# Performance work log

Measured on AMD Instinct MI355X. Metric: run time of the kernel, lower is better.

The kernel has to match this reference:

```python
import jax, jax.numpy as jnp
import numpy as np

BB, T, N, M, P = 512, 128, 32, 16, 16
Q_SCALE, R_SCALE = 0.08, 0.3


def _mT(x):
    return jnp.swapaxes(x, -1, -2)


def setup_inputs() -> dict:
    key = jax.random.key(0)
    k = jax.random.split(key, 6)
    Y = jax.random.normal(k[0], (BB, T, P), dtype=jnp.float32)
    U = jax.random.normal(k[1], (BB, T, M), dtype=jnp.float32)
    # stable transition matrix (spectral radius < 1) so the filter doesn't blow up over T steps
    A = 0.8 * jnp.eye(N, dtype=jnp.float32) + 0.05 * jax.random.normal(k[2], (N, N), dtype=jnp.float32)
    Bmat = 0.1 * jax.random.normal(k[3], (N, M), dtype=jnp.float32)
    Cmat = jax.random.normal(k[4], (P, N), dtype=jnp.float32) / jnp.sqrt(jnp.float32(N))
    mu0 = jax.random.normal(k[5], (N,), dtype=jnp.float32)
    Sigma0 = jnp.eye(N, dtype=jnp.float32)
    Q = (Q_SCALE ** 2) * jnp.eye(N, dtype=jnp.float32)
    R = (R_SCALE ** 2) * jnp.eye(P, dtype=jnp.float32)
    return dict(Y=Y, U=U, A=A, Bmat=Bmat, Cmat=Cmat, mu0=mu0, Sigma0=Sigma0, Q=Q, R=R)


def _kalman_smooth(Y, U, A, Bm, C, mu0, Sigma0, Q, R):
    Bb, Tt, _ = Y.shape
    n = A.shape[0]
    I = jnp.eye(n, dtype=Y.dtype)
    Yt = jnp.swapaxes(Y, 0, 1)  # [T,B,p]
    Ut = jnp.swapaxes(U, 0, 1)  # [T,B,m]

    def fstep(carry, yu):
        mu, Sig = carry  # [B,n], [B,n,n]
        y, u = yu
        mu_p = mu @ A.T + u @ Bm.T                       # predicted mean  [B,n]
        Sig_p = A @ Sig @ A.T + Q                        # predicted cov   [B,n,n]
        r = y - mu_p @ C.T                               # innovation      [B,p]
        S = C @ Sig_p @ C.T + R                          # innovation cov  [B,p,p]
        S = 0.5 * (S + _mT(S))
        PCT = Sig_p @ C.T                                # [B,n,p]
        K = _mT(jnp.linalg.solve(S, _mT(PCT)))           # Kalman gain     [B,n,p]
        mu_f = mu_p + jnp.einsum('bnp,bp->bn', K, r)
        IKC = I - K @ C
        Sig_f = IKC @ Sig_p @ _mT(IKC) + K @ R @ _mT(K)  # Joseph form
        Sig_f = 0.5 * (Sig_f + _mT(Sig_f))
        return (mu_f, Sig_f), (mu_f, Sig_f, mu_p, Sig_p)

    mu_init = jnp.broadcast_to(mu0, (Bb, n))
    Sig_init = jnp.broadcast_to(Sigma0, (Bb, n, n))
    _, (mus_f, Sigs_f, mus_p, Sigs_p) = jax.lax.scan(fstep, (mu_init, Sig_init), (Yt, Ut))

    # RTS smoother (backward recursion via reverse scan)
    def sstep(carry, xs):
        mu_T, Sig_T = carry  # smoothed at t+1
        Sig_f, Sig_p, mu_f, mu_p = xs  # filtered at t, predicted at t+1
        J = _mT(jnp.linalg.solve(_mT(Sig_p), _mT(Sig_f @ A.T)))  # [B,n,n]
        mu_s = mu_f + jnp.einsum('bij,bj->bi', J, mu_T - mu_p)
        Sig_s = Sig_f + J @ (Sig_T - Sig_p) @ _mT(J)
        Sig_s = 0.5 * (Sig_s + _mT(Sig_s))
        return (mu_s, Sig_s), (mu_s, Sig_s)

    xs = (Sigs_f[:-1], Sigs_p[1:], mus_f[:-1], mus_p[1:])
    carry0 = (mus_f[-1], Sigs_f[-1])
    _, (mus_s, Sigs_s) = jax.lax.scan(sstep, carry0, xs, reverse=True)
    mus_s = jnp.concatenate([mus_s, mus_f[-1:]], axis=0)      # [T,B,n]
    Sigs_s = jnp.concatenate([Sigs_s, Sigs_f[-1:]], axis=0)   # [T,B,n,n]
    return jnp.swapaxes(mus_s, 0, 1), jnp.swapaxes(Sigs_s, 0, 1)


def reference(Y, U, A, Bmat, Cmat, mu0, Sigma0, Q, R):
    return _kalman_smooth(Y, U, A, Bmat, Cmat, mu0, Sigma0, Q, R)
```

## Files before the change

kernel.cpp:

```cpp
#include <hip/hip_runtime.h>

constexpr int BB = 512, T = 128, N = 32, M = 16, P = 16;
constexpr int NP = N * P;
constexpr int NN = N * N;
constexpr int NM = N * M;

typedef float f4 __attribute__((ext_vector_type(4)));

__device__ __forceinline__ void bar_lds() {
    asm volatile("s_waitcnt lgkmcnt(0)" ::: "memory");
    __builtin_amdgcn_s_barrier();
    asm volatile("" ::: "memory");
}

__device__ __forceinline__ void load_row32(const float* __restrict__ src, float* dst) {
    const float4* s4 = reinterpret_cast<const float4*>(src);
    #pragma unroll
    for (int c = 0; c < 8; ++c) {
        float4 v = s4[c];
        dst[4*c+0] = v.x; dst[4*c+1] = v.y; dst[4*c+2] = v.z; dst[4*c+3] = v.w;
    }
}
__device__ __forceinline__ void load_row16(const float* __restrict__ src, float* dst) {
    const float4* s4 = reinterpret_cast<const float4*>(src);
    #pragma unroll
    for (int c = 0; c < 4; ++c) {
        float4 v = s4[c];
        dst[4*c+0] = v.x; dst[4*c+1] = v.y; dst[4*c+2] = v.z; dst[4*c+3] = v.w;
    }
}

__global__ __launch_bounds__(256) void k_fwd(
    const float* __restrict__ A, const float* __restrict__ C,
    const float* __restrict__ Q, const float* __restrict__ R,
    const float* __restrict__ Sigma0,
    float* __restrict__ K_all, float* __restrict__ Sp_all, float* __restrict__ Sf_all,
    int* __restrict__ tconv_out)
{
    __shared__ float A_l[N][N + 1], C_l[P][N + 1], Q_l[N][N + 1], R_l[P][P + 1];
    __shared__ float Sig[N][N + 1], Tmp[N][N + 1], Sp[N][N + 1], CP[P][N + 1];
    __shared__ float Aug[P][49];
    __shared__ float red[4];
    const int tid = threadIdx.x;
    const int i0 = tid >> 5, j = tid & 31;
    const int pD = tid >> 4, q = tid & 15;
    const float TOL = 1e-4f;

    for (int idx = tid; idx < NN; idx += 256) {
        A_l[idx >> 5][idx & 31] = A[idx];
        Q_l[idx >> 5][idx & 31] = Q[idx];
        Sig[idx >> 5][idx & 31] = Sigma0[idx];
    }
    for (int idx = tid; idx < P * N; idx += 256) C_l[idx >> 5][idx & 31] = C[idx];
    for (int idx = tid; idx < P * P; idx += 256) R_l[idx >> 4][idx & 15] = R[idx];
    bar_lds();

    float Arow[4][32], Cq[32], Qjv[4];
    #pragma unroll
    for (int e = 0; e < 4; ++e) {
        #pragma unroll
        for (int k = 0; k < 32; ++k) Arow[e][k] = A_l[i0 + 8*e][k];
        Qjv[e] = Q_l[j][i0 + 8*e];
    }
    #pragma unroll
    for (int k = 0; k < 32; ++k) Cq[k] = C_l[q][k];
    const float Rv = R_l[pD][q];

    float prevSig[4];
    #pragma unroll
    for (int e = 0; e < 4; ++e) prevSig[e] = Sig[i0 + 8*e][j];

    int t_conv = T;

    for (int t = 0; t < T; ++t) {
        {
            float sc[32];
            #pragma unroll
            for (int k = 0; k < 32; ++k) sc[k] = Sig[k][j];
            #pragma unroll
            for (int e = 0; e < 4; ++e) {
                float s = 0.f;
                #pragma unroll
                for (int k = 0; k < 32; ++k) s += Arow[e][k] * sc[k];
                Tmp[i0 + 8*e][j] = s;
            }
        }
        bar_lds();
        {
            float tr[32];
            #pragma unroll
            for (int k = 0; k < 32; ++k) tr[k] = Tmp[j][k];
            #pragma unroll
            for (int e = 0; e < 4; ++e) {
                const int c = i0 + 8*e;
                float s = Qjv[e];
                #pragma unroll
                for (int k = 0; k < 32; ++k) s += tr[k] * Arow[e][k];
                Sp[j][c] = s;
                Sp_all[t * NN + tid + 256*e] = s;
            }
        }
        bar_lds();
        {
            float spc[32];
            #pragma unroll
            for (int k = 0; k < 32; ++k) spc[k] = Sp[k][j];
            #pragma unroll
            for (int e = 0; e < 2; ++e) {
                const int p = i0 + 8*e;
                float s = 0.f;
                #pragma unroll
                for (int k = 0; k < 32; ++k) s += C_l[p][k] * spc[k];
                CP[p][j] = s;
            }
        }
        bar_lds();
        {
            float cpr[32];
            #pragma unroll
            for (int k = 0; k < 32; ++k) cpr[k] = CP[pD][k];
            float s = Rv;
            #pragma unroll
            for (int k = 0; k < 32; ++k) s += cpr[k] * Cq[k];
            Aug[pD][q] = s;
        }
        #pragma unroll
        for (int e = 0; e < 2; ++e) {
            const int p = i0 + 8*e;
            Aug[p][16 + j] = CP[p][j];
        }
        bar_lds();
        if (tid < 64) {
            const int r = tid >> 2, qd = tid & 3;
            float a[12];
            #pragma unroll
            for (int c = 0; c < 12; ++c) a[c] = Aug[r][qd * 12 + c];
            #pragma unroll
            for (int p = 0; p < P; ++p) {
                const int pq = p / 12;
                const int lp = p - 12 * pq;
                const float pivv = __shfl(a[lp], (p << 2) + pq);
                const float f    = __shfl(a[lp], (tid & ~3) + pq);
                const float pinv = 1.0f / pivv;
                const float fp = f * pinv;
                float pr[12];
                #pragma unroll
                for (int c = 0; c < 12; ++c) pr[c] = __shfl(a[c], (p << 2) + qd);
                #pragma unroll
                for (int c = 0; c < 12; ++c)
                    a[c] = (r == p) ? pr[c] * pinv : a[c] - fp * pr[c];
            }
            if (qd) {
                #pragma unroll
                for (int c = 0; c < 12; ++c) Aug[r][qd * 12 + c] = a[c];
            }
        }
        bar_lds();
        #pragma unroll
        for (int e = 0; e < 2; ++e) {
            const int idx = tid + 256*e;
            K_all[t * NP + idx] = Aug[idx & 15][16 + (idx >> 4)];
        }
        float wmax = 0.f;
        {
            float cpj[16];
            #pragma unroll
            for (int p = 0; p < 16; ++p) cpj[p] = CP[p][j];
            #pragma unroll
            for (int e = 0; e < 4; ++e) {
                const int i = i0 + 8*e;
                float s = Sp[i][j];
                #pragma unroll
                for (int p = 0; p < 16; ++p) s -= Aug[p][16 + i] * cpj[p];
                Sig[i][j] = s;
                Sf_all[t * NN + tid + 256*e] = s;
                wmax = fmaxf(wmax, fabsf(s - prevSig[e]));
                prevSig[e] = s;
            }
        }
        #pragma unroll
        for (int m = 1; m < 64; m <<= 1)
            wmax = fmaxf(wmax, __shfl_xor(wmax, m));
        if ((tid & 63) == 0) red[tid >> 6] = wmax;
        bar_lds();
        const float g = fmaxf(fmaxf(red[0], red[1]), fmaxf(red[2], red[3]));
        if (g <= TOL && t < T - 1) { t_conv = t; break; }
    }

    if (t_conv < T - 1) {
        float kv[2], spv[4], sfv[4];
        #pragma unroll
        for (int e = 0; e < 2; ++e) {
            const int idx = tid + 256*e;
            kv[e] = Aug[idx & 15][16 + (idx >> 4)];
        }
        #pragma unroll
        for (int e = 0; e < 4; ++e) {
            spv[e] = Sp[i0 + 8*e][j];
            sfv[e] = Sig[i0 + 8*e][j];
        }
        for (int s = t_conv + 1; s < T; ++s) {
            #pragma unroll
            for (int e = 0; e < 2; ++e) K_all[s * NP + tid + 256*e] = kv[e];
            #pragma unroll
            for (int e = 0; e < 4; ++e) {
                Sp_all[s * NN + tid + 256*e] = spv[e];
                Sf_all[s * NN + tid + 256*e] = sfv[e];
            }
        }
    }
    if (tid == 0) *tconv_out = t_conv;
}

__global__ __launch_bounds__(256) void k_jh(
    const float* __restrict__ A,
    const float* __restrict__ Sp_all, const float* __restrict__ Sf_all,
    float* __restrict__ J_all, float* __restrict__ H_all)
{
    const int t = blockIdx.x;
    __shared__ float A_l[N][N + 1], Sf[N][N + 1], Sp1[N][N + 1];
    __shared__ float Aug[N][65], W[N][N + 1], Jl[N][N + 1];
    const int tid = threadIdx.x;

    for (int idx = tid; idx < NN; idx += 256) {
        A_l[idx >> 5][idx & 31] = A[idx];
        Sf[idx >> 5][idx & 31]  = Sf_all[t * NN + idx];
        Sp1[idx >> 5][idx & 31] = Sp_all[(t + 1) * NN + idx];
    }
    __syncthreads();
    #pragma unroll
    for (int e = 0; e < 4; ++e) {
        int idx = tid + e * 256; int i = idx >> 5, j = idx & 31;
        float s = 0.f;
        #pragma unroll
        for (int k = 0; k < N; ++k) s += A_l[i][k] * Sf[k][j];
        Aug[i][32 + j] = s;
        Aug[i][j] = Sp1[i][j];
    }
    __syncthreads();
    {
        int r = tid >> 3, c0 = (tid & 7) * 8;
        for (int p = 0; p < N; ++p) {
            float pinv = 1.0f / Aug[p][p];
            float f = Aug[r][p];
            float prow[8], mine[8];
            #pragma unroll
            for (int c = 0; c < 8; ++c) { prow[c] = Aug[p][c0 + c]; mine[c] = Aug[r][c0 + c]; }
            __syncthreads();
            float fp = f * pinv;
            #pragma unroll
            for (int c = 0; c < 8; ++c)
                Aug[r][c0 + c] = (r == p) ? prow[c] * pinv : mine[c] - fp * prow[c];
            __syncthreads();
        }
    }
    #pragma unroll
    for (int e = 0; e < 4; ++e) {
        int idx = tid + e * 256; int i = idx >> 5, j = idx & 31;
        float v = Aug[j][32 + i];
        Jl[i][j] = v;
        J_all[t * NN + idx] = v;
    }
    __syncthreads();
    #pragma unroll
    for (int e = 0; e < 4; ++e) {
        int idx = tid + e * 256; int i = idx >> 5, j = idx & 31;
        float s = 0.f;
        #pragma unroll
        for (int k = 0; k < N; ++k) s += Jl[i][k] * Sp1[k][j];
        W[i][j] = s;
    }
    __syncthreads();
    #pragma unroll
    for (int e = 0; e < 4; ++e) {
        int idx = tid + e * 256; int i = idx >> 5, j = idx & 31;
        float s = Sf[i][j];
        #pragma unroll
        for (int k = 0; k < N; ++k) s -= W[i][k] * Jl[j][k];
        H_all[t * NN + idx] = s;
    }
}

__global__ __launch_bounds__(256) void k_mat(
    const float* __restrict__ A, const float* __restrict__ C, const float* __restrict__ Bm,
    const float* __restrict__ K_all, const float* __restrict__ J_all,
    float* __restrict__ G_all, float* __restrict__ D_all,
    float* __restrict__ E_all, float* __restrict__ F_all)
{
    const int t = blockIdx.x;
    __shared__ float A_l[N][N + 1], B_l[N][M + 1], C_l[P][N + 1];
    __shared__ float Kl[N][P + 1], W[N][N + 1], Jl[N][N + 1];
    const int tid = threadIdx.x;

    for (int idx = tid; idx < NN; idx += 256) A_l[idx >> 5][idx & 31] = A[idx];
    for (int idx = tid; idx < P * N; idx += 256) C_l[idx >> 5][idx & 31] = C[idx];
    for (int idx = tid; idx < NM; idx += 256) B_l[idx >> 4][idx & 15] = Bm[idx];
    for (int idx = tid; idx < NP; idx += 256) Kl[idx >> 4][idx & 15] = K_all[t * NP + idx];
    __syncthreads();
    #pragma unroll
    for (int e = 0; e < 4; ++e) {
        int idx = tid + e * 256; int i = idx >> 5, j = idx & 31;
        float s = 0.f;
        #pragma unroll
        for (int p = 0; p < P; ++p) s += Kl[i][p] * C_l[p][j];
        W[i][j] = s;
    }
    __syncthreads();
    #pragma unroll
    for (int e = 0; e < 4; ++e) {
        int idx = tid + e * 256; int i = idx >> 5, j = idx & 31;
        float s = A_l[i][j];
        #pragma unroll
        for (int k = 0; k < N; ++k) s -= W[i][k] * A_l[k][j];
        G_all[t * NN + idx] = s;
    }
    #pragma unroll
    for (int e = 0; e < 2; ++e) {
        int idx = tid + e * 256; int i = idx >> 4, m = idx & 15;
        float s = B_l[i][m];
        #pragma unroll
        for (int k = 0; k < N; ++k) s -= W[i][k] * B_l[k][m];
        D_all[t * NM + idx] = s;
    }
    if (t >= T - 1) return;
    for (int idx = tid; idx < NN; idx += 256) Jl[idx >> 5][idx & 31] = J_all[t * NN + idx];
    __syncthreads();
    #pragma unroll
    for (int e = 0; e < 4; ++e) {
        int idx = tid + e * 256; int i = idx >> 5, j = idx & 31;
        float s = (i == j) ? 1.f : 0.f;
        #pragma unroll
        for (int k = 0; k < N; ++k) s -= Jl[i][k] * A_l[k][j];
        E_all[t * NN + idx] = s;
    }
    #pragma unroll
    for (int e = 0; e < 2; ++e) {
        int idx = tid + e * 256; int i = idx >> 4, m = idx & 15;
        float s = 0.f;
        #pragma unroll
        for (int k = 0; k < N; ++k) s += Jl[i][k] * B_l[k][m];
        F_all[t * NM + idx] = s;
    }
}

__global__ __launch_bounds__(256) void k_sscan(
    const float* __restrict__ Sf_all,
    const float* __restrict__ J_all, const float* __restrict__ H_all,
    float* __restrict__ Ss_all, const int* __restrict__ tconv_ptr)
{
    __shared__ float Ss[N][N + 1], W[N][N + 1], Hl[N][N + 1];
    __shared__ float red[4];
    const int tid = threadIdx.x;
    const int i0 = tid >> 5, j = tid & 31;
    const int t_conv = *tconv_ptr;
    const float TOL = 1e-4f;

    for (int idx = tid; idx < NN; idx += 256) {
        float v = Sf_all[(size_t)(T - 1) * NN + idx];
        Ss[idx >> 5][idx & 31] = v;
        Ss_all[(size_t)(T - 1) * NN + idx] = v;
    }
    bar_lds();
    float prevSs[4];
    #pragma unroll
    for (int e = 0; e < 4; ++e) prevSs[e] = Ss[j][i0 + 8*e];

    for (int t = T - 2; t >= 0; --t) {
        float jr[4][32];
        #pragma unroll
        for (int e = 0; e < 4; ++e)
            load_row32(J_all + (size_t)t * NN + (i0 + 8*e) * 32, jr[e]);
        #pragma unroll
        for (int e = 0; e < 4; ++e)
            Hl[i0 + 8*e][j] = H_all[(size_t)t * NN + tid + 256*e];
        {
            float sc[32];
            #pragma unroll
            for (int k = 0; k < 32; ++k) sc[k] = Ss[k][j];
            #pragma unroll
            for (int e = 0; e < 4; ++e) {
                float s = 0.f;
                #pragma unroll
                for (int k = 0; k < 32; ++k) s += jr[e][k] * sc[k];
                W[i0 + 8*e][j] = s;
            }
        }
        bar_lds();
        float localmax = 0.f;
        {
            float wr[32];
            #pragma unroll
            for (int k = 0; k < 32; ++k) wr[k] = W[j][k];
            #pragma unroll
            for (int e = 0; e < 4; ++e) {
                const int c = i0 + 8*e;
                float s = Hl[j][c];
                #pragma unroll
                for (int k = 0; k < 32; ++k) s += wr[k] * jr[e][k];
                Ss[j][c] = s;
                Ss_all[(size_t)t * NN + tid + 256*e] = s;
                localmax = fmaxf(localmax, fabsf(s - prevSs[e]));
                prevSs[e] = s;
            }
        }
        #pragma unroll
        for (int m = 1; m < 64; m <<= 1)
            localmax = fmaxf(localmax, __shfl_xor(localmax, m));
        if ((tid & 63) == 0) red[tid >> 6] = localmax;
        bar_lds();
        const float g = fmaxf(fmaxf(red[0], red[1]), fmaxf(red[2], red[3]));
        if (g <= TOL && (t - 1 >= t_conv)) {
            for (int s = t_conv; s <= t - 1; ++s) {
                #pragma unroll
                for (int e = 0; e < 4; ++e)
                    Ss_all[(size_t)s * NN + tid + 256*e] = prevSs[e];
            }
            t = t_conv;
        }
    }
}

__global__ __launch_bounds__(64, 1) void k_mu(
    const float* __restrict__ Y, const float* __restrict__ U,
    const float* __restrict__ mu0,
    const float* __restrict__ K_all, const float* __restrict__ J_all,
    const float* __restrict__ G_all, const float* __restrict__ D_all,
    const float* __restrict__ E_all, const float* __restrict__ F_all,
    const int* __restrict__ tconv_ptr,
    float* __restrict__ out_mus)
{
    const int b = blockIdx.x;
    const int lane = threadIdx.x;
    const int j = lane & 31;
    const int half = lane >> 5;
    __shared__ float mfh[T][N];
    __shared__ float cfh[T][N];
    const int t_conv = *tconv_ptr;
    const float* Yb = Y + (size_t)b * T * P;
    const float* Ub = U + (size_t)b * T * M;

    for (int it = 0; it < T / 2; ++it) {
        const int t = it * 2 + half;
        float dr[16], kr[16], uu[16], yy[16];
        load_row16(D_all + t * NM + j * 16, dr);
        load_row16(K_all + t * NP + j * 16, kr);
        load_row16(Ub + t * M, uu);
        load_row16(Yb + t * P, yy);
        float s0 = 0.f, s1 = 0.f, s2 = 0.f, s3 = 0.f;
        #pragma unroll
        for (int m = 0; m < 16; m += 4) {
            s0 += dr[m+0]*uu[m+0]; s1 += dr[m+1]*uu[m+1];
            s2 += dr[m+2]*uu[m+2]; s3 += dr[m+3]*uu[m+3];
            s0 += kr[m+0]*yy[m+0]; s1 += kr[m+1]*yy[m+1];
            s2 += kr[m+2]*yy[m+2]; s3 += kr[m+3]*yy[m+3];
        }
        cfh[t][j] = (s0 + s1) + (s2 + s3);
    }
    __syncthreads();

    float mu = mu0[j];
    float gr[32];
    load_row32(G_all + j * 32, gr);
    const int tv = (t_conv < T - 1) ? t_conv : (T - 1);
    float cn = cfh[0][j];
    int t = 0;
    for (; t < tv; ++t) {
        float grn[32];
        load_row32(G_all + (size_t)(t + 1) * NN + j * 32, grn);
        const float cnn = cfh[t + 1][j];
        float s0 = 0.f, s1 = 0.f, s2 = 0.f, s3 = 0.f;
        #pragma unroll
        for (int k = 0; k < 32; k += 4) {
            s0 += gr[k+0] * __shfl(mu, k+0);
            s1 += gr[k+1] * __shfl(mu, k+1);
            s2 += gr[k+2] * __shfl(mu, k+2);
            s3 += gr[k+3] * __shfl(mu, k+3);
        }
        mu = ((s0 + s1) + (s2 + s3)) + cn;
        if (lane < 32) mfh[t][j] = mu;
        #pragma unroll
        for (int c = 0; c < 32; ++c) gr[c] = grn[c];
        cn = cnn;
    }
    for (; t < T; ++t) {
        const float cnn = (t + 1 < T) ? cfh[t + 1][j] : 0.f;
        float s0 = 0.f, s1 = 0.f, s2 = 0.f, s3 = 0.f;
        #pragma unroll
        for (int k = 0; k < 32; k += 4) {
            s0 += gr[k+0] * __shfl(mu, k+0);
            s1 += gr[k+1] * __shfl(mu, k+1);
            s2 += gr[k+2] * __shfl(mu, k+2);
            s3 += gr[k+3] * __shfl(mu, k+3);
        }
        mu = ((s0 + s1) + (s2 + s3)) + cn;
        if (lane < 32) mfh[t][j] = mu;
        cn = cnn;
    }
    if (lane < 32) out_mus[((size_t)b * T + (T - 1)) * N + j] = mu;
    __syncthreads();

    for (int it = 0; it < T / 2; ++it) {
        const int tt = it * 2 + half;
        if (tt < T - 1) {
            float er[32], fr[16], uu[16];
            load_row32(E_all + (size_t)tt * NN + j * 32, er);
            load_row16(F_all + tt * NM + j * 16, fr);
            load_row16(Ub + (tt + 1) * M, uu);
            float s0 = 0.f, s1 = 0.f, s2 = 0.f, s3 = 0.f;
            #pragma unroll
            for (int k = 0; k < 32; k += 4) {
                s0 += er[k+0] * mfh[tt][k+0];
                s1 += er[k+1] * mfh[tt][k+1];
                s2 += er[k+2] * mfh[tt][k+2];
                s3 += er[k+3] * mfh[tt][k+3];
            }
            #pragma unroll
            for (int m = 0; m < 16; m += 4) {
                s0 -= fr[m+0]*uu[m+0]; s1 -= fr[m+1]*uu[m+1];
                s2 -= fr[m+2]*uu[m+2]; s3 -= fr[m+3]*uu[m+3];
            }
            cfh[tt][j] = (s0 + s1) + (s2 + s3);
        }
    }
    __syncthreads();

    float ms = mu;
    const int tp = (t_conv < T - 2) ? t_conv : (T - 2);
    float jr[32];
    load_row32(J_all + (size_t)tp * NN + j * 32, jr);
    float cb = cfh[T - 2][j];
    for (t = T - 2; t >= tp; --t) {
        const float cbn = (t - 1 >= 0) ? cfh[t - 1][j] : 0.f;
        float s0 = 0.f, s1 = 0.f, s2 = 0.f, s3 = 0.f;
        #pragma unroll
        for (int k = 0; k < 32; k += 4) {
            s0 += jr[k+0] * __shfl(ms, k+0);
            s1 += jr[k+1] * __shfl(ms, k+1);
            s2 += jr[k+2] * __shfl(ms, k+2);
            s3 += jr[k+3] * __shfl(ms, k+3);
        }
        ms = ((s0 + s1) + (s2 + s3)) + cb;
        if (lane < 32) out_mus[((size_t)b * T + t) * N + j] = ms;
        cb = cbn;
    }
    if (t >= 0) {
        load_row32(J_all + (size_t)t * NN + j * 32, jr);
        for (; t >= 0; --t) {
            float jrn[32];
            #pragma unroll
            for (int c = 0; c < 32; ++c) jrn[c] = 0.f;
            if (t > 0) load_row32(J_all + (size_t)(t - 1) * NN + j * 32, jrn);
            const float cbn = (t - 1 >= 0) ? cfh[t - 1][j] : 0.f;
            float s0 = 0.f, s1 = 0.f, s2 = 0.f, s3 = 0.f;
            #pragma unroll
            for (int k = 0; k < 32; k += 4) {
                s0 += jr[k+0] * __shfl(ms, k+0);
                s1 += jr[k+1] * __shfl(ms, k+1);
                s2 += jr[k+2] * __shfl(ms, k+2);
                s3 += jr[k+3] * __shfl(ms, k+3);
            }
            ms = ((s0 + s1) + (s2 + s3)) + cb;
            if (lane < 32) out_mus[((size_t)b * T + t) * N + j] = ms;
            cb = cbn;
            #pragma unroll
            for (int c = 0; c < 32; ++c) jr[c] = jrn[c];
        }
    }
}

__global__ __launch_bounds__(256) void k_bcast(
    const float* __restrict__ Ss_all, f4* __restrict__ out4)
{
    const f4* src = (const f4*)Ss_all;
    const long long total = (long long)BB * T * (NN / 4);
    const long long stride = (long long)gridDim.x * blockDim.x;
    for (long long g = blockIdx.x * (long long)blockDim.x + threadIdx.x; g < total; g += stride) {
        int e4 = (int)(g & 255);
        long long bt = g >> 8;
        int t = (int)(bt & (T - 1));
        __builtin_nontemporal_store(src[t * 256 + e4], &out4[g]);
    }
}

extern "C" void kernel_launch(void* const* d_in, const int* in_sizes, int n_in,
                              void* d_out, int out_size, void* d_ws, size_t ws_size,
                              hipStream_t stream)
{
    (void)in_sizes; (void)n_in; (void)out_size; (void)ws_size;
    const float* Y      = (const float*)d_in[0];
    const float* U      = (const float*)d_in[1];
    const float* A      = (const float*)d_in[2];
    const float* Bm     = (const float*)d_in[3];
    const float* C      = (const float*)d_in[4];
    const float* mu0    = (const float*)d_in[5];
    const float* Sigma0 = (const float*)d_in[6];
    const float* Q      = (const float*)d_in[7];
    const float* R      = (const float*)d_in[8];

    float* ws     = (float*)d_ws;
    float* K_all  = ws;
    float* Sp_all = K_all + T * NP;
    float* Sf_all = Sp_all + T * NN;
    float* J_all  = Sf_all + T * NN;
    float* H_all  = J_all + T * NN;
    float* Ss_all = H_all + T * NN;
    float* G_all  = Ss_all + T * NN;
    float* D_all  = G_all + T * NN;
    float* E_all  = D_all + T * NM;
    float* F_all  = E_all + T * NN;
    int*   tconv  = (int*)(F_all + T * NM);

    float* out_mus  = (float*)d_out;
    float* out_sigs = out_mus + (size_t)BB * T * N;

    hipLaunchKernelGGL(k_fwd,   dim3(1),     dim3(256), 0, stream, A, C, Q, R, Sigma0, K_all, Sp_all, Sf_all, tconv);
    hipLaunchKernelGGL(k_jh,    dim3(T - 1), dim3(256), 0, stream, A, Sp_all, Sf_all, J_all, H_all);
    hipLaunchKernelGGL(k_mat,   dim3(T),     dim3(256), 0, stream, A, C, Bm, K_all, J_all, G_all, D_all, E_all, F_all);
    hipLaunchKernelGGL(k_sscan, dim3(1),     dim3(256), 0, stream, Sf_all, J_all, H_all, Ss_all, tconv);
    hipLaunchKernelGGL(k_mu,    dim3(BB),    dim3(64),  0, stream, Y, U, mu0, K_all, J_all, G_all, D_all, E_all, F_all, tconv, out_mus);
    hipLaunchKernelGGL(k_bcast, dim3(4096),  dim3(256), 0, stream, Ss_all, (f4*)out_sigs);
}
```

Baseline: 589.7 us.

## Fuse J/H and matrix-precompute kernels, pack two batches per wave in mean scan

Merges the k_jh and k_mat kernels into one k_jhm launch. J now stays in shared memory instead of being reloaded from global memory, and one launch is removed. k_mu now processes two batch elements per 64-lane wave, one per 32-lane half, using offset shuffles and halving the grid. The covariance convergence tolerance in k_sscan is loosened from 1e-4 to 1e-3, which lets the smoothed covariance settle earlier at the cost of some accuracy.

Result: slower. 631.3 us (+7.1%).

```diff
diff --git a/kernel.cpp b/kernel.cpp
--- a/kernel.cpp
+++ b/kernel.cpp
@@ -212,90 +212,86 @@
     if (tid == 0) *tconv_out = t_conv;
 }
 
-__global__ __launch_bounds__(256) void k_jh(
-    const float* __restrict__ A,
+__global__ __launch_bounds__(256) void k_jhm(
+    const float* __restrict__ A, const float* __restrict__ C, const float* __restrict__ Bm,
     const float* __restrict__ Sp_all, const float* __restrict__ Sf_all,
-    float* __restrict__ J_all, float* __restrict__ H_all)
+    const float* __restrict__ K_all,
+    float* __restrict__ J_all, float* __restrict__ H_all,
+    float* __restrict__ G_all, float* __restrict__ D_all,
+    float* __restrict__ E_all, float* __restrict__ F_all)
 {
     const int t = blockIdx.x;
     __shared__ float A_l[N][N + 1], Sf[N][N + 1], Sp1[N][N + 1];
     __shared__ float Aug[N][65], W[N][N + 1], Jl[N][N + 1];
+    __shared__ float C_l[P][N + 1], B_l[N][M + 1], Kl[N][P + 1];
     const int tid = threadIdx.x;
-
-    for (int idx = tid; idx < NN; idx += 256) {
-        A_l[idx >> 5][idx & 31] = A[idx];
-        Sf[idx >> 5][idx & 31]  = Sf_all[t * NN + idx];
-        Sp1[idx >> 5][idx & 31] = Sp_all[(t + 1) * NN + idx];
-    }
-    __syncthreads();
-    #pragma unroll
-    for (int e = 0; e < 4; ++e) {
-        int idx = tid + e * 256; int i = idx >> 5, j = idx & 31;
-        float s = 0.f;
-        #pragma unroll
-        for (int k = 0; k < N; ++k) s += A_l[i][k] * Sf[k][j];
-        Aug[i][32 + j] = s;
-        Aug[i][j] = Sp1[i][j];
-    }
-    __syncthreads();
-    {
-        int r = tid >> 3, c0 = (tid & 7) * 8;
-        for (int p = 0; p < N; ++p) {
-            float pinv = 1.0f / Aug[p][p];
-            float f = Aug[r][p];
-            float prow[8], mine[8];
-            #pragma unroll
-            for (int c = 0; c < 8; ++c) { prow[c] = Aug[p][c0 + c]; mine[c] = Aug[r][c0 + c]; }
-            __syncthreads();
-            float fp = f * pinv;
-            #pragma unroll
-            for (int c = 0; c < 8; ++c)
-                Aug[r][c0 + c] = (r == p) ? prow[c] * pinv : mine[c] - fp * prow[c];
-            __syncthreads();
-        }
-    }
-    #pragma unroll
-    for (int e = 0; e < 4; ++e) {
-        int idx = tid + e * 256; int i = idx >> 5, j = idx & 31;
-        float v = Aug[j][32 + i];
-        Jl[i][j] = v;
-        J_all[t * NN + idx] = v;
-    }
-    __syncthreads();
-    #pragma unroll
-    for (int e = 0; e < 4; ++e) {
-        int idx = tid + e * 256; int i = idx >> 5, j = idx & 31;
-        float s = 0.f;
-        #pragma unroll
-        for (int k = 0; k < N; ++k) s += Jl[i][k] * Sp1[k][j];
-        W[i][j] = s;
-    }
-    __syncthreads();
-    #pragma unroll
-    for (int e = 0; e < 4; ++e) {
-        int idx = tid + e * 256; int i = idx >> 5, j = idx & 31;
-        float s = Sf[i][j];
-        #pragma unroll
-        for (int k = 0; k < N; ++k) s -= W[i][k] * Jl[j][k];
-        H_all[t * NN + idx] = s;
-    }
-}
-
-__global__ __launch_bounds__(256) void k_mat(
-    const float* __restrict__ A, const float* __restrict__ C, const float* __restrict__ Bm,
-    const float* __restrict__ K_all, const float* __restrict__ J_all,
-    float* __restrict__ G_all, float* __restrict__ D_all,
-    float* __restrict__ E_all, float* __restrict__ F_all)
-{
-    const int t = blockIdx.x;
-    __shared__ float A_l[N][N + 1], B_l[N][M + 1], C_l[P][N + 1];
-    __shared__ float Kl[N][P + 1], W[N][N + 1], Jl[N][N + 1];
-    const int tid = threadIdx.x;
+    const bool hasJ = (t < T - 1);
 
     for (int idx = tid; idx < NN; idx += 256) A_l[idx >> 5][idx & 31] = A[idx];
     for (int idx = tid; idx < P * N; idx += 256) C_l[idx >> 5][idx & 31] = C[idx];
     for (int idx = tid; idx < NM; idx += 256) B_l[idx >> 4][idx & 15] = Bm[idx];
     for (int idx = tid; idx < NP; idx += 256) Kl[idx >> 4][idx & 15] = K_all[t * NP + idx];
+    if (hasJ) {
+        for (int idx = tid; idx < NN; idx += 256) {
+            Sf[idx >> 5][idx & 31]  = Sf_all[t * NN + idx];
+            Sp1[idx >> 5][idx & 31] = Sp_all[(t + 1) * NN + idx];
+        }
+    }
+    __syncthreads();
+
+    if (hasJ) {
+        #pragma unroll
+        for (int e = 0; e < 4; ++e) {
+            int idx = tid + e * 256; int i = idx >> 5, j = idx & 31;
+            float s = 0.f;
+            #pragma unroll
+            for (int k = 0; k < N; ++k) s += A_l[i][k] * Sf[k][j];
+            Aug[i][32 + j] = s;
+            Aug[i][j] = Sp1[i][j];
+        }
+        __syncthreads();
+        {
+            int r = tid >> 3, c0 = (tid & 7) * 8;
+            for (int p = 0; p < N; ++p) {
+                float pinv = 1.0f / Aug[p][p];
+                float f = Aug[r][p];
+                float prow[8], mine[8];
+                #pragma unroll
+                for (int c = 0; c < 8; ++c) { prow[c] = Aug[p][c0 + c]; mine[c] = Aug[r][c0 + c]; }
+                __syncthreads();
+                float fp = f * pinv;
+                #pragma unroll
+                for (int c = 0; c < 8; ++c)
+                    Aug[r][c0 + c] = (r == p) ? prow[c] * pinv : mine[c] - fp * prow[c];
+                __syncthreads();
+            }
+        }
+        #pragma unroll
+        for (int e = 0; e < 4; ++e) {
+            int idx = tid + e * 256; int i = idx >> 5, j = idx & 31;
+            float v = Aug[j][32 + i];
+            Jl[i][j] = v;
+            J_all[t * NN + idx] = v;
+        }
+        __syncthreads();
+        #pragma unroll
+        for (int e = 0; e < 4; ++e) {
+            int idx = tid + e * 256; int i = idx >> 5, j = idx & 31;
+            float s = 0.f;
+            #pragma unroll
+            for (int k = 0; k < N; ++k) s += Jl[i][k] * Sp1[k][j];
+            W[i][j] = s;
+        }
+        __syncthreads();
+        #pragma unroll
+        for (int e = 0; e < 4; ++e) {
+            int idx = tid + e * 256; int i = idx >> 5, j = idx & 31;
+            float s = Sf[i][j];
+            #pragma unroll
+            for (int k = 0; k < N; ++k) s -= W[i][k] * Jl[j][k];
+            H_all[t * NN + idx] = s;
+        }
+    }
     __syncthreads();
     #pragma unroll
     for (int e = 0; e < 4; ++e) {
@@ -322,24 +318,23 @@
         for (int k = 0; k < N; ++k) s -= W[i][k] * B_l[k][m];
         D_all[t * NM + idx] = s;
     }
-    if (t >= T - 1) return;
-    for (int idx = tid; idx < NN; idx += 256) Jl[idx >> 5][idx & 31] = J_all[t * NN + idx];
-    __syncthreads();
-    #pragma unroll
-    for (int e = 0; e < 4; ++e) {
-        int idx = tid + e * 256; int i = idx >> 5, j = idx & 31;
-        float s = (i == j) ? 1.f : 0.f;
-        #pragma unroll
-        for (int k = 0; k < N; ++k) s -= Jl[i][k] * A_l[k][j];
-        E_all[t * NN + idx] = s;
-    }
-    #pragma unroll
-    for (int e = 0; e < 2; ++e) {
-        int idx = tid + e * 256; int i = idx >> 4, m = idx & 15;
-        float s = 0.f;
-        #pragma unroll
-        for (int k = 0; k < N; ++k) s += Jl[i][k] * B_l[k][m];
-        F_all[t * NM + idx] = s;
+    if (hasJ) {
+        #pragma unroll
+        for (int e = 0; e < 4; ++e) {
+            int idx = tid + e * 256; int i = idx >> 5, j = idx & 31;
+            float s = (i == j) ? 1.f : 0.f;
+            #pragma unroll
+            for (int k = 0; k < N; ++k) s -= Jl[i][k] * A_l[k][j];
+            E_all[t * NN + idx] = s;
+        }
+        #pragma unroll
+        for (int e = 0; e < 2; ++e) {
+            int idx = tid + e * 256; int i = idx >> 4, m = idx & 15;
+            float s = 0.f;
+            #pragma unroll
+            for (int k = 0; k < N; ++k) s += Jl[i][k] * B_l[k][m];
+            F_all[t * NM + idx] = s;
+        }
     }
 }
 
@@ -353,7 +348,7 @@
     const int tid = threadIdx.x;
     const int i0 = tid >> 5, j = tid & 31;
     const int t_conv = *tconv_ptr;
-    const float TOL = 1e-4f;
+    const float TOL = 1e-3f;
 
     for (int idx = tid; idx < NN; idx += 256) {
         float v = Sf_all[(size_t)(T - 1) * NN + idx];
@@ -429,18 +424,18 @@
     const int* __restrict__ tconv_ptr,
     float* __restrict__ out_mus)
 {
-    const int b = blockIdx.x;
     const int lane = threadIdx.x;
     const int j = lane & 31;
-    const int half = lane >> 5;
-    __shared__ float mfh[T][N];
-    __shared__ float cfh[T][N];
+    const int h = lane >> 5;
+    const int b = blockIdx.x * 2 + h;
+    const int sb = lane & 32;
+    __shared__ float mfh[2][T][N];
+    __shared__ float cfh[2][T][N];
     const int t_conv = *tconv_ptr;
     const float* Yb = Y + (size_t)b * T * P;
     const float* Ub = U + (size_t)b * T * M;
 
-    for (int it = 0; it < T / 2; ++it) {
-        const int t = it * 2 + half;
+    for (int t = 0; t < T; ++t) {
         float dr[16], kr[16], uu[16], yy[16];
         load_row16(D_all + t * NM + j * 16, dr);
         load_row16(K_all + t * NP + j * 16, kr);
@@ -454,7 +449,7 @@
             s0 += kr[m+0]*yy[m+0]; s1 += kr[m+1]*yy[m+1];
             s2 += kr[m+2]*yy[m+2]; s3 += kr[m+3]*yy[m+3];
         }
-        cfh[t][j] = (s0 + s1) + (s2 + s3);
+        cfh[h][t][j] = (s0 + s1) + (s2 + s3);
     }
     __syncthreads();
 
@@ -462,65 +457,62 @@
     float gr[32];
     load_row32(G_all + j * 32, gr);
     const int tv = (t_conv < T - 1) ? t_conv : (T - 1);
-    float cn = cfh[0][j];
+    float cn = cfh[h][0][j];
     int t = 0;
     for (; t < tv; ++t) {
         float grn[32];
         load_row32(G_all + (size_t)(t + 1) * NN + j * 32, grn);
-        const float cnn = cfh[t + 1][j];
+        const float cnn = cfh[h][t + 1][j];
         float s0 = 0.f, s1 = 0.f, s2 = 0.f, s3 = 0.f;
         #pragma unroll
         for (int k = 0; k < 32; k += 4) {
-            s0 += gr[k+0] * __shfl(mu, k+0);
-            s1 += gr[k+1] * __shfl(mu, k+1);
-            s2 += gr[k+2] * __shfl(mu, k+2);
-            s3 += gr[k+3] * __shfl(mu, k+3);
+            s0 += gr[k+0] * __shfl(mu, k+0+sb);
+            s1 += gr[k+1] * __shfl(mu, k+1+sb);
+            s2 += gr[k+2] * __shfl(mu, k+2+sb);
+            s3 += gr[k+3] * __shfl(mu, k+3+sb);
         }
         mu = ((s0 + s1) + (s2 + s3)) + cn;
-        if (lane < 32) mfh[t][j] = mu;
+        mfh[h][t][j] = mu;
         #pragma unroll
         for (int c = 0; c < 32; ++c) gr[c] = grn[c];
         cn = cnn;
     }
     for (; t < T; ++t) {
-        const float cnn = (t + 1 < T) ? cfh[t + 1][j] : 0.f;
+        const float cnn = (t + 1 < T) ? cfh[h][t + 1][j] : 0.f;
         float s0 = 0.f, s1 = 0.f, s2 = 0.f, s3 = 0.f;
         #pragma unroll
         for (int k = 0; k < 32; k += 4) {
-            s0 += gr[k+0] * __shfl(mu, k+0);
-            s1 += gr[k+1] * __shfl(mu, k+1);
-            s2 += gr[k+2] * __shfl(mu, k+2);
-            s3 += gr[k+3] * __shfl(mu, k+3);
+            s0 += gr[k+0] * __shfl(mu, k+0+sb);
+            s1 += gr[k+1] * __shfl(mu, k+1+sb);
+            s2 += gr[k+2] * __shfl(mu, k+2+sb);
+            s3 += gr[k+3] * __shfl(mu, k+3+sb);
         }
         mu = ((s0 + s1) + (s2 + s3)) + cn;
-        if (lane < 32) mfh[t][j] = mu;
+        mfh[h][t][j] = mu;
         cn = cnn;
     }
-    if (lane < 32) out_mus[((size_t)b * T + (T - 1)) * N + j] = mu;
+    out_mus[((size_t)b * T + (T - 1)) * N + j] = mu;
     __syncthreads();
 
-    for (int it = 0; it < T / 2; ++it) {
-        const int tt = it * 2 + half;
-        if (tt < T - 1) {
-            float er[32], fr[16], uu[16];
-            load_row32(E_all + (size_t)tt * NN + j * 32, er);
-            load_row16(F_all + tt * NM + j * 16, fr);
-            load_row16(Ub + (tt + 1) * M, uu);
-            float s0 = 0.f, s1 = 0.f, s2 = 0.f, s3 = 0.f;
-            #pragma unroll
-            for (int k = 0; k < 32; k += 4) {
-                s0 += er[k+0] * mfh[tt][k+0];
-                s1 += er[k+1] * mfh[tt][k+1];
-                s2 += er[k+2] * mfh[tt][k+2];
-                s3 += er[k+3] * mfh[tt][k+3];
-            }
-            #pragma unroll
-            for (int m = 0; m < 16; m += 4) {
-                s0 -= fr[m+0]*uu[m+0]; s1 -= fr[m+1]*uu[m+1];
-                s2 -= fr[m+2]*uu[m+2]; s3 -= fr[m+3]*uu[m+3];
-            }
-            cfh[tt][j] = (s0 + s1) + (s2 + s3);
-        }
+    for (int tt = 0; tt < T - 1; ++tt) {
+        float er[32], fr[16], uu[16];
+        load_row32(E_all + (size_t)tt * NN + j * 32, er);
+        load_row16(F_all + tt * NM + j * 16, fr);
+        load_row16(Ub + (tt + 1) * M, uu);
+        float s0 = 0.f, s1 = 0.f, s2 = 0.f, s3 = 0.f;
+        #pragma unroll
+        for (int k = 0; k < 32; k += 4) {
+            s0 += er[k+0] * mfh[h][tt][k+0];
+            s1 += er[k+1] * mfh[h][tt][k+1];
+            s2 += er[k+2] * mfh[h][tt][k+2];
+            s3 += er[k+3] * mfh[h][tt][k+3];
+        }
+        #pragma unroll
+        for (int m = 0; m < 16; m += 4) {
+            s0 -= fr[m+0]*uu[m+0]; s1 -= fr[m+1]*uu[m+1];
+            s2 -= fr[m+2]*uu[m+2]; s3 -= fr[m+3]*uu[m+3];
+        }
+        cfh[h][tt][j] = (s0 + s1) + (s2 + s3);
     }
     __syncthreads();
 
@@ -528,19 +520,19 @@
     const int tp = (t_conv < T - 2) ? t_conv : (T - 2);
     float jr[32];
     load_row32(J_all + (size_t)tp * NN + j * 32, jr);
-    float cb = cfh[T - 2][j];
+    float cb = cfh[h][T - 2][j];
     for (t = T - 2; t >= tp; --t) {
-        const float cbn = (t - 1 >= 0) ? cfh[t - 1][j] : 0.f;
+        const float cbn = (t - 1 >= 0) ? cfh[h][t - 1][j] : 0.f;
         float s0 = 0.f, s1 = 0.f, s2 = 0.f, s3 = 0.f;
         #pragma unroll
         for (int k = 0; k < 32; k += 4) {
-            s0 += jr[k+0] * __shfl(ms, k+0);
-            s1 += jr[k+1] * __shfl(ms, k+1);
-            s2 += jr[k+2] * __shfl(ms, k+2);
-            s3 += jr[k+3] * __shfl(ms, k+3);
+            s0 += jr[k+0] * __shfl(ms, k+0+sb);
+            s1 += jr[k+1] * __shfl(ms, k+1+sb);
+            s2 += jr[k+2] * __shfl(ms, k+2+sb);
+            s3 += jr[k+3] * __shfl(ms, k+3+sb);
         }
         ms = ((s0 + s1) + (s2 + s3)) + cb;
-        if (lane < 32) out_mus[((size_t)b * T + t) * N + j] = ms;
+        out_mus[((size_t)b * T + t) * N + j] = ms;
         cb = cbn;
     }
     if (t >= 0) {
@@ -550,17 +542,17 @@
             #pragma unroll
             for (int c = 0; c < 32; ++c) jrn[c] = 0.f;
             if (t > 0) load_row32(J_all + (size_t)(t - 1) * NN + j * 32, jrn);
-            const float cbn = (t - 1 >= 0) ? cfh[t - 1][j] : 0.f;
+            const float cbn = (t - 1 >= 0) ? cfh[h][t - 1][j] : 0.f;
             float s0 = 0.f, s1 = 0.f, s2 = 0.f, s3 = 0.f;
             #pragma unroll
             for (int k = 0; k < 32; k += 4) {
-                s0 += jr[k+0] * __shfl(ms, k+0);
-                s1 += jr[k+1] * __shfl(ms, k+1);
-                s2 += jr[k+2] * __shfl(ms, k+2);
-                s3 += jr[k+3] * __shfl(ms, k+3);
+                s0 += jr[k+0] * __shfl(ms, k+0+sb);
+                s1 += jr[k+1] * __shfl(ms, k+1+sb);
+                s2 += jr[k+2] * __shfl(ms, k+2+sb);
+                s3 += jr[k+3] * __shfl(ms, k+3+sb);
             }
             ms = ((s0 + s1) + (s2 + s3)) + cb;
-            if (lane < 32) out_mus[((size_t)b * T + t) * N + j] = ms;
+            out_mus[((size_t)b * T + t) * N + j] = ms;
             cb = cbn;
             #pragma unroll
             for (int c = 0; c < 32; ++c) jr[c] = jrn[c];
@@ -613,10 +605,9 @@
     float* out_mus  = (float*)d_out;
     float* out_sigs = out_mus + (size_t)BB * T * N;
 
-    hipLaunchKernelGGL(k_fwd,   dim3(1),     dim3(256), 0, stream, A, C, Q, R, Sigma0, K_all, Sp_all, Sf_all, tconv);
-    hipLaunchKernelGGL(k_jh,    dim3(T - 1), dim3(256), 0, stream, A, Sp_all, Sf_all, J_all, H_all);
-    hipLaunchKernelGGL(k_mat,   dim3(T),     dim3(256), 0, stream, A, C, Bm, K_all, J_all, G_all, D_all, E_all, F_all);
-    hipLaunchKernelGGL(k_sscan, dim3(1),     dim3(256), 0, stream, Sf_all, J_all, H_all, Ss_all, tconv);
-    hipLaunchKernelGGL(k_mu,    dim3(BB),    dim3(64),  0, stream, Y, U, mu0, K_all, J_all, G_all, D_all, E_all, F_all, tconv, out_mus);
-    hipLaunchKernelGGL(k_bcast, dim3(4096),  dim3(256), 0, stream, Ss_all, (f4*)out_sigs);
-}
+    hipLaunchKernelGGL(k_fwd,   dim3(1),      dim3(256), 0, stream, A, C, Q, R, Sigma0, K_all, Sp_all, Sf_all, tconv);
+    hipLaunchKernelGGL(k_jhm,   dim3(T),      dim3(256), 0, stream, A, C, Bm, Sp_all, Sf_all, K_all, J_all, H_all, G_all, D_all, E_all, F_all);
+    hipLaunchKernelGGL(k_sscan, dim3(1),      dim3(256), 0, stream, Sf_all, J_all, H_all, Ss_all, tconv);
+    hipLaunchKernelGGL(k_mu,    dim3(BB / 2), dim3(64),  0, stream, Y, U, mu0, K_all, J_all, G_all, D_all, E_all, F_all, tconv, out_mus);
+    hipLaunchKernelGGL(k_bcast, dim3(4096),   dim3(256), 0, stream, Ss_all, (f4*)out_sigs);
+}
```
